# Kernel tuning notes

Measured on AMD Instinct MI355X. Metric: run time of the kernel, lower is better.

## Reference

```python
import jax, jax.numpy as jnp
import numpy as np

# --- module hyperparameters (from init_kwargs) ---
B, C, LEN_TS = 256, 8, 4096
K = 128                      # shapelet / kernel length
DIM = 3                      # channel selected by shapelet_info[5]
WINDOW = 1024
START = max(0, 1000 - WINDOW)          # 0
END = min(LEN_TS, 1128 + WINDOW)       # 2152
OUT = END - START - K + 1              # 2025 sliding windows
NORM = 10.0
ALPHA = -10.0
BNORM = 100.0
MAX_CI = 3.0
MAX_NORM_DIST = 1e-5                   # non-trainable buffer (initial value)


def setup_inputs() -> dict:
    key = jax.random.key(0)
    k1, k2 = jax.random.split(key)
    x = jax.random.normal(k1, (B, C, LEN_TS), dtype=jnp.float32)
    shapelet = jax.random.normal(k2, (1, K), dtype=jnp.float32)
    return {"x": x, "shapelet": shapelet, "ep": 1}


def reference(x, shapelet, ep):
    # ep != 0 / eval mode: the max_norm_dist buffer-update branch is skipped.
    sh = shapelet[0]                                  # [K]
    sh_d = jax.lax.stop_gradient(sh)                  # torch uses .data.detach() for CI
    ci_sh = jnp.sum(jnp.square(sh_d[1:] - sh_d[:-1])) + 1.0 / NORM  # scalar

    pis = x[:, DIM, START:END]                        # [B, L], L = END-START
    d2 = jnp.square(pis[:, 1:] - pis[:, :-1])         # [B, L-1] squared diffs

    # windowed sum of K-1 consecutive squared diffs via cumulative sum
    zero = jnp.zeros((pis.shape[0], 1), pis.dtype)
    cs = jnp.concatenate([zero, jnp.cumsum(d2, axis=1)], axis=1)   # [B, L]
    ci_pis = cs[:, K - 1:K - 1 + OUT] - cs[:, :OUT] + 1.0 / NORM   # [B, OUT]

    # complexity-invariance correction, clipped at MAX_CI
    ci_dist = jnp.minimum(jnp.maximum(ci_pis, ci_sh) / jnp.minimum(ci_pis, ci_sh), MAX_CI)

    # sliding windows of the series (torch unfold)
    idx = jnp.arange(OUT)[:, None] + jnp.arange(K)[None, :]        # [OUT, K]
    win = pis[:, idx]                                              # [B, OUT, K]

    # normalized CI-corrected L2 shapelet distance per window
    dist = jnp.sum(jnp.square(win - sh), axis=2) * ci_dist / K     # [B, OUT]

    # exp-weighted soft minimum over windows
    d = dist / BNORM
    w = jnp.exp(ALPHA * d)
    softmin = (jnp.sum(w * d, axis=1, keepdims=True)
               / jnp.sum(w, axis=1, keepdims=True)) * BNORM        # [B, 1]

    return 1.0 - softmin / MAX_NORM_DIST
```

## Files before the change

kernel.cpp:

```cpp
#include <hip/hip_runtime.h>
#include <math.h>

constexpr int B       = 256;
constexpr int C       = 8;
constexpr int LEN_TS  = 4096;
constexpr int K       = 128;
constexpr int DIM     = 3;
constexpr int START   = 0;
constexpr int END     = 2152;
constexpr int PIS_LEN = END - START;
constexpr int OUTW    = PIS_LEN - K + 1;
constexpr float INV_NORM      = 0.1f;
constexpr float ALPHA         = -10.0f;
constexpr float BNORM         = 100.0f;
constexpr float MAX_CI        = 3.0f;
constexpr float MAX_NORM_DIST = 1e-5f;

constexpr int TPB     = 512;
constexpr int NWAVES  = TPB / 64;
constexpr int PIS_PAD = 2176;

__global__ __launch_bounds__(TPB)
void pis_dist_block_kernel(const float* __restrict__ x,
                           const float* __restrict__ shapelet,
                           float* __restrict__ out) {
    __shared__ __align__(16) float s_pis[PIS_PAD];
    __shared__ float s_red[2][NWAVES];

    const int b    = blockIdx.x;
    const int tid  = threadIdx.x;
    const int lane = tid & 63;

    const float* xrow = x + ((size_t)b * C + DIM) * LEN_TS + START;
    const float4* xr4 = reinterpret_cast<const float4*>(xrow);
    float4* sp4 = reinterpret_cast<float4*>(s_pis);
    for (int i = tid; i < PIS_LEN / 4; i += TPB) sp4[i] = xr4[i];
    if (tid < (PIS_PAD - PIS_LEN)) s_pis[PIS_LEN + tid] = 0.0f;

    float ci_sh;
    {
        float a0 = shapelet[lane];
        float a1 = shapelet[lane + 1];
        float c  = (a1 - a0) * (a1 - a0);
        if (lane < 63) {
            float b0 = shapelet[lane + 64];
            float b1 = shapelet[lane + 65];
            c = fmaf(b1 - b0, b1 - b0, c);
        }
        #pragma unroll
        for (int off = 32; off; off >>= 1) c += __shfl_xor(c, off);
        ci_sh = c + INV_NORM;
    }
    __syncthreads();

    const float4* shg = reinterpret_cast<const float4*>(shapelet);
    const float4* pis4 = reinterpret_cast<const float4*>(s_pis);
    const int t = tid;

    float s0 = 0.f, s1 = 0.f, s2 = 0.f, s3 = 0.f;
    float cs = 0.f;

    float4 pc = pis4[t];
    float4 sc = shg[0];
    const float f0 = pc.x, f1 = pc.y, f2 = pc.z, f3 = pc.w;

    {
        float d, dd;
        d  = pc.x - sc.x; s0 = fmaf(d, d, s0);
        dd = pc.y - pc.x; cs = fmaf(dd, dd, cs);
        d  = pc.y - sc.y; s0 = fmaf(d, d, s0);
        d  = pc.y - sc.x; s1 = fmaf(d, d, s1);
        dd = pc.z - pc.y; cs = fmaf(dd, dd, cs);
        d  = pc.z - sc.z; s0 = fmaf(d, d, s0);
        d  = pc.z - sc.y; s1 = fmaf(d, d, s1);
        d  = pc.z - sc.x; s2 = fmaf(d, d, s2);
        dd = pc.w - pc.z; cs = fmaf(dd, dd, cs);
        d  = pc.w - sc.w; s0 = fmaf(d, d, s0);
        d  = pc.w - sc.z; s1 = fmaf(d, d, s1);
        d  = pc.w - sc.y; s2 = fmaf(d, d, s2);
        d  = pc.w - sc.x; s3 = fmaf(d, d, s3);
    }

    #pragma unroll 4
    for (int i = 1; i < 32; ++i) {
        float4 pp = pis4[t + i];
        float4 ss = shg[i];
        float d, dd;
        dd = pp.x - pc.w; cs = fmaf(dd, dd, cs);
        d = pp.x - ss.x; s0 = fmaf(d, d, s0);
        d = pp.x - sc.w; s1 = fmaf(d, d, s1);
        d = pp.x - sc.z; s2 = fmaf(d, d, s2);
        d = pp.x - sc.y; s3 = fmaf(d, d, s3);
        dd = pp.y - pp.x; cs = fmaf(dd, dd, cs);
        d = pp.y - ss.y; s0 = fmaf(d, d, s0);
        d = pp.y - ss.x; s1 = fmaf(d, d, s1);
        d = pp.y - sc.w; s2 = fmaf(d, d, s2);
        d = pp.y - sc.z; s3 = fmaf(d, d, s3);
        dd = pp.z - pp.y; cs = fmaf(dd, dd, cs);
        d = pp.z - ss.z; s0 = fmaf(d, d, s0);
        d = pp.z - ss.y; s1 = fmaf(d, d, s1);
        d = pp.z - ss.x; s2 = fmaf(d, d, s2);
        d = pp.z - sc.w; s3 = fmaf(d, d, s3);
        dd = pp.w - pp.z; cs = fmaf(dd, dd, cs);
        d = pp.w - ss.w; s0 = fmaf(d, d, s0);
        d = pp.w - ss.z; s1 = fmaf(d, d, s1);
        d = pp.w - ss.y; s2 = fmaf(d, d, s2);
        d = pp.w - ss.x; s3 = fmaf(d, d, s3);
        pc = pp; sc = ss;
    }

    float4 pl = pis4[t + 32];
    {
        float d;
        d = pl.x - sc.w; s1 = fmaf(d, d, s1);
        d = pl.x - sc.z; s2 = fmaf(d, d, s2);
        d = pl.x - sc.y; s3 = fmaf(d, d, s3);
        d = pl.y - sc.w; s2 = fmaf(d, d, s2);
        d = pl.y - sc.z; s3 = fmaf(d, d, s3);
        d = pl.z - sc.w; s3 = fmaf(d, d, s3);
    }

    float d2a = (f1 - f0) * (f1 - f0);
    float d2b = (f2 - f1) * (f2 - f1);
    float d2c = (f3 - f2) * (f3 - f2);
    float e0 = (pl.x - pc.w) * (pl.x - pc.w);
    float e1 = (pl.y - pl.x) * (pl.y - pl.x);
    float e2 = (pl.z - pl.y) * (pl.z - pl.y);
    float sd0 = cs;
    float sd1 = sd0 - d2a + e0;
    float sd2 = sd1 - d2b + e1;
    float sd3 = sd2 - d2c + e2;

    float wd_sum = 0.f, w_sum = 0.f;
    const int o0 = 4 * t;
    {
        float mx, mn, ci, cid, dist, dv, wt;
        if (o0 + 0 < OUTW) {
            ci = sd0 + INV_NORM; mx = fmaxf(ci, ci_sh); mn = fminf(ci, ci_sh);
            cid = fminf(mx / mn, MAX_CI);
            dist = s0 * cid * (1.0f / (float)K); dv = dist * (1.0f / BNORM);
            wt = __expf(ALPHA * dv); wd_sum = fmaf(wt, dv, wd_sum); w_sum += wt;
        }
        if (o0 + 1 < OUTW) {
            ci = sd1 + INV_NORM; mx = fmaxf(ci, ci_sh); mn = fminf(ci, ci_sh);
            cid = fminf(mx / mn, MAX_CI);
            dist = s1 * cid * (1.0f / (float)K); dv = dist * (1.0f / BNORM);
            wt = __expf(ALPHA * dv); wd_sum = fmaf(wt, dv, wd_sum); w_sum += wt;
        }
        if (o0 + 2 < OUTW) {
            ci = sd2 + INV_NORM; mx = fmaxf(ci, ci_sh); mn = fminf(ci, ci_sh);
            cid = fminf(mx / mn, MAX_CI);
            dist = s2 * cid * (1.0f / (float)K); dv = dist * (1.0f / BNORM);
            wt = __expf(ALPHA * dv); wd_sum = fmaf(wt, dv, wd_sum); w_sum += wt;
        }
        if (o0 + 3 < OUTW) {
            ci = sd3 + INV_NORM; mx = fmaxf(ci, ci_sh); mn = fminf(ci, ci_sh);
            cid = fminf(mx / mn, MAX_CI);
            dist = s3 * cid * (1.0f / (float)K); dv = dist * (1.0f / BNORM);
            wt = __expf(ALPHA * dv); wd_sum = fmaf(wt, dv, wd_sum); w_sum += wt;
        }
    }

    #pragma unroll
    for (int off = 32; off; off >>= 1) {
        wd_sum += __shfl_down(wd_sum, off);
        w_sum  += __shfl_down(w_sum, off);
    }
    const int wv = tid >> 6;
    if (lane == 0) {
        s_red[0][wv] = wd_sum;
        s_red[1][wv] = w_sum;
    }
    __syncthreads();
    if (tid == 0) {
        float wd = 0.f, wt = 0.f;
        #pragma unroll
        for (int i = 0; i < NWAVES; ++i) {
            wd += s_red[0][i];
            wt += s_red[1][i];
        }
        float softmin = wd / wt * BNORM;
        out[b] = 1.0f - softmin / MAX_NORM_DIST;
    }
}

extern "C" void kernel_launch(void* const* d_in, const int* in_sizes, int n_in,
                              void* d_out, int out_size, void* d_ws, size_t ws_size,
                              hipStream_t stream) {
    const float* x        = (const float*)d_in[0];
    const float* shapelet = (const float*)d_in[1];
    float* out            = (float*)d_out;
    pis_dist_block_kernel<<<B, TPB, 0, stream>>>(x, shapelet, out);
}
```

Measured before the change: 11.47 us.

## Split each series across two blocks and expand squared distance into dot products

Each batch row is now processed by two 256-thread blocks, each covering half of the windows. The partial sums go to workspace and a second small kernel combines them. The squared-distance and complexity sums are rewritten as dot products (||p||^2 - 2p·s + ||s||^2), which cuts per-element subtractions. This adds an extra kernel launch and a workspace round trip, and cancellation in the expanded form may lose accuracy. A dead leftover block kernel that no longer computes anything useful is also left in the file.

```diff
diff --git a/kernel.cpp b/kernel.cpp
--- a/kernel.cpp
+++ b/kernel.cpp
@@ -6,9 +6,7 @@
 constexpr int LEN_TS  = 4096;
 constexpr int K       = 128;
 constexpr int DIM     = 3;
-constexpr int START   = 0;
-constexpr int END     = 2152;
-constexpr int PIS_LEN = END - START;
+constexpr int PIS_LEN = 2152;
 constexpr int OUTW    = PIS_LEN - K + 1;
 constexpr float INV_NORM      = 0.1f;
 constexpr float ALPHA         = -10.0f;
@@ -16,147 +14,154 @@
 constexpr float MAX_CI        = 3.0f;
 constexpr float MAX_NORM_DIST = 1e-5f;
 
-constexpr int TPB     = 512;
+constexpr int TPB     = 256;
 constexpr int NWAVES  = TPB / 64;
-constexpr int PIS_PAD = 2176;
+constexpr int WPB     = 4 * TPB;
+constexpr int NHALF   = 2;
+constexpr int NSTAGE4 = TPB + 32;
 
 __global__ __launch_bounds__(TPB)
 void pis_dist_block_kernel(const float* __restrict__ x,
                            const float* __restrict__ shapelet,
                            float* __restrict__ out) {
-    __shared__ __align__(16) float s_pis[PIS_PAD];
+    __shared__ __align__(16) float s_pis[NSTAGE4 * 4];
     __shared__ float s_red[2][NWAVES];
 
-    const int b    = blockIdx.x;
+    const int blk  = blockIdx.x;
+    const int b    = blk >> 1;
+    const int h    = blk & 1;
     const int tid  = threadIdx.x;
     const int lane = tid & 63;
 
-    const float* xrow = x + ((size_t)b * C + DIM) * LEN_TS + START;
-    const float4* xr4 = reinterpret_cast<const float4*>(xrow);
+    const float4* xr4 = reinterpret_cast<const float4*>(
+                            x + ((size_t)b * C + DIM) * LEN_TS) + (size_t)h * (WPB / 4);
     float4* sp4 = reinterpret_cast<float4*>(s_pis);
-    for (int i = tid; i < PIS_LEN / 4; i += TPB) sp4[i] = xr4[i];
-    if (tid < (PIS_PAD - PIS_LEN)) s_pis[PIS_LEN + tid] = 0.0f;
-
-    float ci_sh;
+    for (int i = tid; i < NSTAGE4; i += TPB) sp4[i] = xr4[i];
+
+    float ci_sh, SH2;
     {
         float a0 = shapelet[lane];
         float a1 = shapelet[lane + 1];
-        float c  = (a1 - a0) * (a1 - a0);
+        float b0 = shapelet[lane + 64];
+        float cci  = (a1 - a0) * (a1 - a0);
+        float csh2 = fmaf(a0, a0, b0 * b0);
         if (lane < 63) {
-            float b0 = shapelet[lane + 64];
             float b1 = shapelet[lane + 65];
-            c = fmaf(b1 - b0, b1 - b0, c);
+            cci = fmaf(b1 - b0, b1 - b0, cci);
         }
         #pragma unroll
-        for (int off = 32; off; off >>= 1) c += __shfl_xor(c, off);
-        ci_sh = c + INV_NORM;
+        for (int off = 32; off; off >>= 1) {
+            cci  += __shfl_xor(cci,  off);
+            csh2 += __shfl_xor(csh2, off);
+        }
+        ci_sh = cci + INV_NORM;
+        SH2   = csh2;
     }
     __syncthreads();
 
-    const float4* shg = reinterpret_cast<const float4*>(shapelet);
+    const float4* shg  = reinterpret_cast<const float4*>(shapelet);
     const float4* pis4 = reinterpret_cast<const float4*>(s_pis);
     const int t = tid;
 
-    float s0 = 0.f, s1 = 0.f, s2 = 0.f, s3 = 0.f;
-    float cs = 0.f;
+    float X0 = 0.f, X1 = 0.f, X2 = 0.f, X3 = 0.f;
+    float cp = 0.f;
+    float cc = 0.f;
 
     float4 pc = pis4[t];
     float4 sc = shg[0];
     const float f0 = pc.x, f1 = pc.y, f2 = pc.z, f3 = pc.w;
 
     {
-        float d, dd;
-        d  = pc.x - sc.x; s0 = fmaf(d, d, s0);
-        dd = pc.y - pc.x; cs = fmaf(dd, dd, cs);
-        d  = pc.y - sc.y; s0 = fmaf(d, d, s0);
-        d  = pc.y - sc.x; s1 = fmaf(d, d, s1);
-        dd = pc.z - pc.y; cs = fmaf(dd, dd, cs);
-        d  = pc.z - sc.z; s0 = fmaf(d, d, s0);
-        d  = pc.z - sc.y; s1 = fmaf(d, d, s1);
-        d  = pc.z - sc.x; s2 = fmaf(d, d, s2);
-        dd = pc.w - pc.z; cs = fmaf(dd, dd, cs);
-        d  = pc.w - sc.w; s0 = fmaf(d, d, s0);
-        d  = pc.w - sc.z; s1 = fmaf(d, d, s1);
-        d  = pc.w - sc.y; s2 = fmaf(d, d, s2);
-        d  = pc.w - sc.x; s3 = fmaf(d, d, s3);
+        X0 = fmaf(pc.x, sc.x, X0);
+        X0 = fmaf(pc.y, sc.y, X0); X1 = fmaf(pc.y, sc.x, X1);
+        X0 = fmaf(pc.z, sc.z, X0); X1 = fmaf(pc.z, sc.y, X1);
+        X2 = fmaf(pc.z, sc.x, X2);
+        X0 = fmaf(pc.w, sc.w, X0); X1 = fmaf(pc.w, sc.z, X1);
+        X2 = fmaf(pc.w, sc.y, X2); X3 = fmaf(pc.w, sc.x, X3);
+        cp = fmaf(pc.x, pc.x, cp); cp = fmaf(pc.y, pc.y, cp);
+        cp = fmaf(pc.z, pc.z, cp); cp = fmaf(pc.w, pc.w, cp);
+        cc = fmaf(pc.y, pc.x, cc);
+        cc = fmaf(pc.z, pc.y, cc);
+        cc = fmaf(pc.w, pc.z, cc);
     }
 
     #pragma unroll 4
     for (int i = 1; i < 32; ++i) {
         float4 pp = pis4[t + i];
         float4 ss = shg[i];
-        float d, dd;
-        dd = pp.x - pc.w; cs = fmaf(dd, dd, cs);
-        d = pp.x - ss.x; s0 = fmaf(d, d, s0);
-        d = pp.x - sc.w; s1 = fmaf(d, d, s1);
-        d = pp.x - sc.z; s2 = fmaf(d, d, s2);
-        d = pp.x - sc.y; s3 = fmaf(d, d, s3);
-        dd = pp.y - pp.x; cs = fmaf(dd, dd, cs);
-        d = pp.y - ss.y; s0 = fmaf(d, d, s0);
-        d = pp.y - ss.x; s1 = fmaf(d, d, s1);
-        d = pp.y - sc.w; s2 = fmaf(d, d, s2);
-        d = pp.y - sc.z; s3 = fmaf(d, d, s3);
-        dd = pp.z - pp.y; cs = fmaf(dd, dd, cs);
-        d = pp.z - ss.z; s0 = fmaf(d, d, s0);
-        d = pp.z - ss.y; s1 = fmaf(d, d, s1);
-        d = pp.z - ss.x; s2 = fmaf(d, d, s2);
-        d = pp.z - sc.w; s3 = fmaf(d, d, s3);
-        dd = pp.w - pp.z; cs = fmaf(dd, dd, cs);
-        d = pp.w - ss.w; s0 = fmaf(d, d, s0);
-        d = pp.w - ss.z; s1 = fmaf(d, d, s1);
-        d = pp.w - ss.y; s2 = fmaf(d, d, s2);
-        d = pp.w - ss.x; s3 = fmaf(d, d, s3);
+        cc = fmaf(pp.x, pc.w, cc);
+        X0 = fmaf(pp.x, ss.x, X0); X1 = fmaf(pp.x, sc.w, X1);
+        X2 = fmaf(pp.x, sc.z, X2); X3 = fmaf(pp.x, sc.y, X3);
+        cp = fmaf(pp.x, pp.x, cp);
+        cc = fmaf(pp.y, pp.x, cc);
+        X0 = fmaf(pp.y, ss.y, X0); X1 = fmaf(pp.y, ss.x, X1);
+        X2 = fmaf(pp.y, sc.w, X2); X3 = fmaf(pp.y, sc.z, X3);
+        cp = fmaf(pp.y, pp.y, cp);
+        cc = fmaf(pp.z, pp.y, cc);
+        X0 = fmaf(pp.z, ss.z, X0); X1 = fmaf(pp.z, ss.y, X1);
+        X2 = fmaf(pp.z, ss.x, X2); X3 = fmaf(pp.z, sc.w, X3);
+        cp = fmaf(pp.z, pp.z, cp);
+        cc = fmaf(pp.w, pp.z, cc);
+        X0 = fmaf(pp.w, ss.w, X0); X1 = fmaf(pp.w, ss.z, X1);
+        X2 = fmaf(pp.w, ss.y, X2); X3 = fmaf(pp.w, ss.x, X3);
+        cp = fmaf(pp.w, pp.w, cp);
         pc = pp; sc = ss;
     }
 
     float4 pl = pis4[t + 32];
     {
-        float d;
-        d = pl.x - sc.w; s1 = fmaf(d, d, s1);
-        d = pl.x - sc.z; s2 = fmaf(d, d, s2);
-        d = pl.x - sc.y; s3 = fmaf(d, d, s3);
-        d = pl.y - sc.w; s2 = fmaf(d, d, s2);
-        d = pl.y - sc.z; s3 = fmaf(d, d, s3);
-        d = pl.z - sc.w; s3 = fmaf(d, d, s3);
-    }
-
+        X1 = fmaf(pl.x, sc.w, X1);
+        X2 = fmaf(pl.x, sc.z, X2); X2 = fmaf(pl.y, sc.w, X2);
+        X3 = fmaf(pl.x, sc.y, X3); X3 = fmaf(pl.y, sc.z, X3);
+        X3 = fmaf(pl.z, sc.w, X3);
+    }
+
+    const float p127 = pc.w;
+    float sp2_0 = cp;
+    float sp2_1 = sp2_0 - f0 * f0 + pl.x * pl.x;
+    float sp2_2 = sp2_1 - f1 * f1 + pl.y * pl.y;
+    float sp2_3 = sp2_2 - f2 * f2 + pl.z * pl.z;
+    float ss0 = sp2_0 - 2.f * X0 + SH2;
+    float ss1 = sp2_1 - 2.f * X1 + SH2;
+    float ss2 = sp2_2 - 2.f * X2 + SH2;
+    float ss3 = sp2_3 - 2.f * X3 + SH2;
     float d2a = (f1 - f0) * (f1 - f0);
     float d2b = (f2 - f1) * (f2 - f1);
     float d2c = (f3 - f2) * (f3 - f2);
-    float e0 = (pl.x - pc.w) * (pl.x - pc.w);
-    float e1 = (pl.y - pl.x) * (pl.y - pl.x);
-    float e2 = (pl.z - pl.y) * (pl.z - pl.y);
-    float sd0 = cs;
+    float e0  = (pl.x - p127) * (pl.x - p127);
+    float e1  = (pl.y - pl.x) * (pl.y - pl.x);
+    float e2  = (pl.z - pl.y) * (pl.z - pl.y);
+    float sd0 = (cp - f0 * f0) + (cp - p127 * p127) - 2.f * cc;
     float sd1 = sd0 - d2a + e0;
     float sd2 = sd1 - d2b + e1;
     float sd3 = sd2 - d2c + e2;
 
     float wd_sum = 0.f, w_sum = 0.f;
-    const int o0 = 4 * t;
+    const int og = h * WPB + 4 * t;
     {
         float mx, mn, ci, cid, dist, dv, wt;
-        if (o0 + 0 < OUTW) {
+        if (og + 0 < OUTW) {
             ci = sd0 + INV_NORM; mx = fmaxf(ci, ci_sh); mn = fminf(ci, ci_sh);
             cid = fminf(mx / mn, MAX_CI);
-            dist = s0 * cid * (1.0f / (float)K); dv = dist * (1.0f / BNORM);
-            wt = __expf(ALPHA * dv); wd_sum = fmaf(wt, dv, wd_sum); w_sum += wt;
-        }
-        if (o0 + 1 < OUTW) {
+            dist = ss0 * cid * (1.0f / (float)K); dv = dist * (1.0f / BNORM);
+            wt = __expf(ALPHA * dv); wd_sum = fmaf(wt, dv, wd_sum); w_sum += wt;
+        }
+        if (og + 1 < OUTW) {
             ci = sd1 + INV_NORM; mx = fmaxf(ci, ci_sh); mn = fminf(ci, ci_sh);
             cid = fminf(mx / mn, MAX_CI);
-            dist = s1 * cid * (1.0f / (float)K); dv = dist * (1.0f / BNORM);
-            wt = __expf(ALPHA * dv); wd_sum = fmaf(wt, dv, wd_sum); w_sum += wt;
-        }
-        if (o0 + 2 < OUTW) {
+            dist = ss1 * cid * (1.0f / (float)K); dv = dist * (1.0f / BNORM);
+            wt = __expf(ALPHA * dv); wd_sum = fmaf(wt, dv, wd_sum); w_sum += wt;
+        }
+        if (og + 2 < OUTW) {
             ci = sd2 + INV_NORM; mx = fmaxf(ci, ci_sh); mn = fminf(ci, ci_sh);
             cid = fminf(mx / mn, MAX_CI);
-            dist = s2 * cid * (1.0f / (float)K); dv = dist * (1.0f / BNORM);
-            wt = __expf(ALPHA * dv); wd_sum = fmaf(wt, dv, wd_sum); w_sum += wt;
-        }
-        if (o0 + 3 < OUTW) {
+            dist = ss2 * cid * (1.0f / (float)K); dv = dist * (1.0f / BNORM);
+            wt = __expf(ALPHA * dv); wd_sum = fmaf(wt, dv, wd_sum); w_sum += wt;
+        }
+        if (og + 3 < OUTW) {
             ci = sd3 + INV_NORM; mx = fmaxf(ci, ci_sh); mn = fminf(ci, ci_sh);
             cid = fminf(mx / mn, MAX_CI);
-            dist = s3 * cid * (1.0f / (float)K); dv = dist * (1.0f / BNORM);
+            dist = ss3 * cid * (1.0f / (float)K); dv = dist * (1.0f / BNORM);
             wt = __expf(ALPHA * dv); wd_sum = fmaf(wt, dv, wd_sum); w_sum += wt;
         }
     }
@@ -173,12 +178,192 @@
     }
     __syncthreads();
     if (tid == 0) {
-        float wd = 0.f, wt = 0.f;
+        float wd = s_red[0][0] + s_red[0][1] + s_red[0][2] + s_red[0][3];
+        float wt = s_red[1][0] + s_red[1][1] + s_red[1][2] + s_red[1][3];
+        atomicAdd(&out[2 * b + 0], 0.0f);
+        (void)wd; (void)wt;
+    }
+    if (tid == 0) {
+        float wd = s_red[0][0] + s_red[0][1] + s_red[0][2] + s_red[0][3];
+        float wt = s_red[1][0] + s_red[1][1] + s_red[1][2] + s_red[1][3];
+        float* ws = reinterpret_cast<float*>(out) + B;
+        (void)ws;
+        wd_sum = wd; w_sum = wt;
+    }
+}
+
+
+__global__ __launch_bounds__(TPB)
+void pis_dist_half_kernel(const float* __restrict__ x,
+                          const float* __restrict__ shapelet,
+                          float* __restrict__ partial) {
+    __shared__ __align__(16) float s_pis[NSTAGE4 * 4];
+    __shared__ float s_red[2][NWAVES];
+
+    const int blk  = blockIdx.x;
+    const int b    = blk >> 1;
+    const int h    = blk & 1;
+    const int tid  = threadIdx.x;
+    const int lane = tid & 63;
+
+    const float4* xr4 = reinterpret_cast<const float4*>(
+                            x + ((size_t)b * C + DIM) * LEN_TS) + (size_t)h * (WPB / 4);
+    float4* sp4 = reinterpret_cast<float4*>(s_pis);
+    for (int i = tid; i < NSTAGE4; i += TPB) sp4[i] = xr4[i];
+
+    float ci_sh, SH2;
+    {
+        float a0 = shapelet[lane];
+        float a1 = shapelet[lane + 1];
+        float b0 = shapelet[lane + 64];
+        float cci  = (a1 - a0) * (a1 - a0);
+        float csh2 = fmaf(a0, a0, b0 * b0);
+        if (lane < 63) {
+            float b1 = shapelet[lane + 65];
+            cci = fmaf(b1 - b0, b1 - b0, cci);
+        }
         #pragma unroll
-        for (int i = 0; i < NWAVES; ++i) {
-            wd += s_red[0][i];
-            wt += s_red[1][i];
-        }
+        for (int off = 32; off; off >>= 1) {
+            cci  += __shfl_xor(cci,  off);
+            csh2 += __shfl_xor(csh2, off);
+        }
+        ci_sh = cci + INV_NORM;
+        SH2   = csh2;
+    }
+    __syncthreads();
+
+    const float4* shg  = reinterpret_cast<const float4*>(shapelet);
+    const float4* pis4 = reinterpret_cast<const float4*>(s_pis);
+    const int t = tid;
+
+    float X0 = 0.f, X1 = 0.f, X2 = 0.f, X3 = 0.f;
+    float cp = 0.f, cc = 0.f;
+
+    float4 pc = pis4[t];
+    float4 sc = shg[0];
+    const float f0 = pc.x, f1 = pc.y, f2 = pc.z, f3 = pc.w;
+
+    {
+        X0 = fmaf(pc.x, sc.x, X0);
+        X0 = fmaf(pc.y, sc.y, X0); X1 = fmaf(pc.y, sc.x, X1);
+        X0 = fmaf(pc.z, sc.z, X0); X1 = fmaf(pc.z, sc.y, X1);
+        X2 = fmaf(pc.z, sc.x, X2);
+        X0 = fmaf(pc.w, sc.w, X0); X1 = fmaf(pc.w, sc.z, X1);
+        X2 = fmaf(pc.w, sc.y, X2); X3 = fmaf(pc.w, sc.x, X3);
+        cp = fmaf(pc.x, pc.x, cp); cp = fmaf(pc.y, pc.y, cp);
+        cp = fmaf(pc.z, pc.z, cp); cp = fmaf(pc.w, pc.w, cp);
+        cc = fmaf(pc.y, pc.x, cc);
+        cc = fmaf(pc.z, pc.y, cc);
+        cc = fmaf(pc.w, pc.z, cc);
+    }
+
+    #pragma unroll 4
+    for (int i = 1; i < 32; ++i) {
+        float4 pp = pis4[t + i];
+        float4 ss = shg[i];
+        cc = fmaf(pp.x, pc.w, cc);
+        X0 = fmaf(pp.x, ss.x, X0); X1 = fmaf(pp.x, sc.w, X1);
+        X2 = fmaf(pp.x, sc.z, X2); X3 = fmaf(pp.x, sc.y, X3);
+        cp = fmaf(pp.x, pp.x, cp);
+        cc = fmaf(pp.y, pp.x, cc);
+        X0 = fmaf(pp.y, ss.y, X0); X1 = fmaf(pp.y, ss.x, X1);
+        X2 = fmaf(pp.y, sc.w, X2); X3 = fmaf(pp.y, sc.z, X3);
+        cp = fmaf(pp.y, pp.y, cp);
+        cc = fmaf(pp.z, pp.y, cc);
+        X0 = fmaf(pp.z, ss.z, X0); X1 = fmaf(pp.z, ss.y, X1);
+        X2 = fmaf(pp.z, ss.x, X2); X3 = fmaf(pp.z, sc.w, X3);
+        cp = fmaf(pp.z, pp.z, cp);
+        cc = fmaf(pp.w, pp.z, cc);
+        X0 = fmaf(pp.w, ss.w, X0); X1 = fmaf(pp.w, ss.z, X1);
+        X2 = fmaf(pp.w, ss.y, X2); X3 = fmaf(pp.w, ss.x, X3);
+        cp = fmaf(pp.w, pp.w, cp);
+        pc = pp; sc = ss;
+    }
+
+    float4 pl = pis4[t + 32];
+    {
+        X1 = fmaf(pl.x, sc.w, X1);
+        X2 = fmaf(pl.x, sc.z, X2); X2 = fmaf(pl.y, sc.w, X2);
+        X3 = fmaf(pl.x, sc.y, X3); X3 = fmaf(pl.y, sc.z, X3);
+        X3 = fmaf(pl.z, sc.w, X3);
+    }
+
+    const float p127 = pc.w;
+    float sp2_0 = cp;
+    float sp2_1 = sp2_0 - f0 * f0 + pl.x * pl.x;
+    float sp2_2 = sp2_1 - f1 * f1 + pl.y * pl.y;
+    float sp2_3 = sp2_2 - f2 * f2 + pl.z * pl.z;
+    float ss0 = sp2_0 - 2.f * X0 + SH2;
+    float ss1 = sp2_1 - 2.f * X1 + SH2;
+    float ss2 = sp2_2 - 2.f * X2 + SH2;
+    float ss3 = sp2_3 - 2.f * X3 + SH2;
+    float d2a = (f1 - f0) * (f1 - f0);
+    float d2b = (f2 - f1) * (f2 - f1);
+    float d2c = (f3 - f2) * (f3 - f2);
+    float e0  = (pl.x - p127) * (pl.x - p127);
+    float e1  = (pl.y - pl.x) * (pl.y - pl.x);
+    float e2  = (pl.z - pl.y) * (pl.z - pl.y);
+    float sd0 = (cp - f0 * f0) + (cp - p127 * p127) - 2.f * cc;
+    float sd1 = sd0 - d2a + e0;
+    float sd2 = sd1 - d2b + e1;
+    float sd3 = sd2 - d2c + e2;
+
+    float wd_sum = 0.f, w_sum = 0.f;
+    const int og = h * WPB + 4 * t;
+    {
+        float mx, mn, ci, cid, dist, dv, wt;
+        if (og + 0 < OUTW) {
+            ci = sd0 + INV_NORM; mx = fmaxf(ci, ci_sh); mn = fminf(ci, ci_sh);
+            cid = fminf(mx / mn, MAX_CI);
+            dist = ss0 * cid * (1.0f / (float)K); dv = dist * (1.0f / BNORM);
+            wt = __expf(ALPHA * dv); wd_sum = fmaf(wt, dv, wd_sum); w_sum += wt;
+        }
+        if (og + 1 < OUTW) {
+            ci = sd1 + INV_NORM; mx = fmaxf(ci, ci_sh); mn = fminf(ci, ci_sh);
+            cid = fminf(mx / mn, MAX_CI);
+            dist = ss1 * cid * (1.0f / (float)K); dv = dist * (1.0f / BNORM);
+            wt = __expf(ALPHA * dv); wd_sum = fmaf(wt, dv, wd_sum); w_sum += wt;
+        }
+        if (og + 2 < OUTW) {
+            ci = sd2 + INV_NORM; mx = fmaxf(ci, ci_sh); mn = fminf(ci, ci_sh);
+            cid = fminf(mx / mn, MAX_CI);
+            dist = ss2 * cid * (1.0f / (float)K); dv = dist * (1.0f / BNORM);
+            wt = __expf(ALPHA * dv); wd_sum = fmaf(wt, dv, wd_sum); w_sum += wt;
+        }
+        if (og + 3 < OUTW) {
+            ci = sd3 + INV_NORM; mx = fmaxf(ci, ci_sh); mn = fminf(ci, ci_sh);
+            cid = fminf(mx / mn, MAX_CI);
+            dist = ss3 * cid * (1.0f / (float)K); dv = dist * (1.0f / BNORM);
+            wt = __expf(ALPHA * dv); wd_sum = fmaf(wt, dv, wd_sum); w_sum += wt;
+        }
+    }
+
+    #pragma unroll
+    for (int off = 32; off; off >>= 1) {
+        wd_sum += __shfl_down(wd_sum, off);
+        w_sum  += __shfl_down(w_sum, off);
+    }
+    const int wv = tid >> 6;
+    if (lane == 0) {
+        s_red[0][wv] = wd_sum;
+        s_red[1][wv] = w_sum;
+    }
+    __syncthreads();
+    if (tid == 0) {
+        float wd = s_red[0][0] + s_red[0][1] + s_red[0][2] + s_red[0][3];
+        float wt = s_red[1][0] + s_red[1][1] + s_red[1][2] + s_red[1][3];
+        partial[(2 * b + h) * 2 + 0] = wd;
+        partial[(2 * b + h) * 2 + 1] = wt;
+    }
+}
+
+__global__ __launch_bounds__(256)
+void pis_finish_kernel(const float* __restrict__ partial,
+                       float* __restrict__ out) {
+    const int b = blockIdx.x * blockDim.x + threadIdx.x;
+    if (b < B) {
+        float wd = partial[(2 * b) * 2 + 0] + partial[(2 * b + 1) * 2 + 0];
+        float wt = partial[(2 * b) * 2 + 1] + partial[(2 * b + 1) * 2 + 1];
         float softmin = wd / wt * BNORM;
         out[b] = 1.0f - softmin / MAX_NORM_DIST;
     }
@@ -190,5 +375,7 @@
     const float* x        = (const float*)d_in[0];
     const float* shapelet = (const float*)d_in[1];
     float* out            = (float*)d_out;
-    pis_dist_block_kernel<<<B, TPB, 0, stream>>>(x, shapelet, out);
+    float* partial        = (float*)d_ws;
+    pis_dist_half_kernel<<<B * NHALF, TPB, 0, stream>>>(x, shapelet, partial);
+    pis_finish_kernel<<<1, 256, 0, stream>>>(partial, out);
 }
```

Result: slower. 13.06 us (+13.8%).
